# Kernel optimization log

Measured on AMD Instinct MI355X. Metric: run time of the kernel, lower is better.

## Reference

```python
import jax, jax.numpy as jnp
import numpy as np
import math

E_IN, E_OUT = 512, 96
B, QL, PL = 64, 128, 196

def _lin(k, shape):
    fan_in = shape[1]
    bound = 1.0 / math.sqrt(fan_in)
    k1, k2 = jax.random.split(k)
    W = jax.random.uniform(k1, shape, jnp.float32, -bound, bound)
    b = jax.random.uniform(k2, (shape[0],), jnp.float32, -bound, bound)
    return W, b

def setup_inputs() -> dict:
    key = jax.random.key(0)
    ks = jax.random.split(key, 16)
    inp = {
        'z_d_cls': jax.random.normal(ks[0], (B, E_IN), jnp.float32),
        'Z_d_tok': jax.random.normal(ks[1], (B, QL, E_IN), jnp.float32),
        'z_t_cls': jax.random.normal(ks[2], (B, E_IN), jnp.float32),
        'Z_t_tok': jax.random.normal(ks[3], (B, QL, E_IN), jnp.float32),
        'z_v_cls': jax.random.normal(ks[4], (B, E_IN), jnp.float32),
        'Z_v_patch': jax.random.normal(ks[5], (B, PL, E_IN), jnp.float32),
    }
    names = ['t_cls', 'd_cls', 'v_cls', 't_tok', 'v_patch', 'tgl_q', 'tgl_k', 'tgl_v']
    for i, n in enumerate(names):
        W, b = _lin(ks[6 + i], (E_OUT, E_IN))
        inp[f'W_{n}'] = W
        inp[f'b_{n}'] = b
    inp['ln_g'] = jnp.ones((E_OUT,), jnp.float32)
    inp['ln_b'] = jnp.zeros((E_OUT,), jnp.float32)
    return inp

def _l2n(x, eps=1e-6):
    return x / jnp.maximum(jnp.linalg.norm(x, axis=-1, keepdims=True), eps)

def _proj(x, W, b):
    return x @ W.T + b

def _layer_norm(x, g, b, eps=1e-5):
    mu = jnp.mean(x, axis=-1, keepdims=True)
    var = jnp.mean((x - mu) ** 2, axis=-1, keepdims=True)
    return (x - mu) / jnp.sqrt(var + eps) * g + b

def reference(z_d_cls, Z_d_tok, z_t_cls, Z_t_tok, z_v_cls, Z_v_patch,
              W_t_cls, b_t_cls, W_d_cls, b_d_cls, W_v_cls, b_v_cls,
              W_t_tok, b_t_tok, W_v_patch, b_v_patch,
              W_tgl_q, b_tgl_q, W_tgl_k, b_tgl_k, W_tgl_v, b_tgl_v,
              ln_g, ln_b):
    # --- TGG: global-global text/doc cosine sim [B, B]
    t = _l2n(_proj(z_t_cls, W_t_cls, b_t_cls))
    d = _l2n(_proj(z_d_cls, W_d_cls, b_d_cls))
    S_TGG = t @ d.T
    # --- TGL: cross-attention over all batch pairs
    Q = _proj(Z_d_tok, W_tgl_q, b_tgl_q)   # [b, q, h]
    K = _proj(Z_t_tok, W_tgl_k, b_tgl_k)   # [c, k, h]
    V = _proj(Z_t_tok, W_tgl_v, b_tgl_v)   # [c, k, h]
    scores = jnp.einsum('bqh,ckh->bcqk', Q, K) / math.sqrt(E_OUT)
    attn = jax.nn.softmax(scores, axis=-1)
    context = jnp.einsum('bcqk,ckh->bcqh', attn, V).mean(axis=2)  # [b, c, h]
    context = _layer_norm(context, ln_g, ln_b)
    S_TGL = jnp.einsum('ih,ijh->ij', d, _l2n(context))
    S_TIB = 0.5 * (S_TGG + S_TGL)
    # --- CGG: global-global text/vision cosine sim
    v = _l2n(_proj(z_v_cls, W_v_cls, b_v_cls))
    S_CGG = t @ v.T
    # --- CLL: token-patch max similarity
    t_tok = _l2n(_proj(Z_t_tok, W_t_tok, b_t_tok))        # [b, t, h]
    v_pat = _l2n(_proj(Z_v_patch, W_v_patch, b_v_patch))  # [c, p, h]
    sim = jnp.einsum('bth,cph->bctp', t_tok, v_pat)
    S_CLL = sim.max(axis=(-1, -2))
    S_CAB = 0.5 * (S_CGG + S_CLL)
    return S_TIB + S_CAB
```

## Files before the change

kernel.cpp:

```cpp
#include <hip/hip_runtime.h>
#include <hip/hip_bf16.h>
#include <math.h>

typedef __bf16 bf16;
typedef __attribute__((ext_vector_type(8))) __bf16 bf16x8;
typedef __attribute__((ext_vector_type(4))) float f32x4;
typedef __attribute__((ext_vector_type(4))) unsigned int uint4v;

#define MFMA16(a, b, c) __builtin_amdgcn_mfma_f32_16x16x32_bf16(a, b, c, 0, 0, 0)

#define QSCALE 0.14724450f

__device__ inline bf16x8 cvt8(const float* p) {
    f32x4 lo = *(const f32x4*)p;
    f32x4 hi = *(const f32x4*)(p + 4);
    bf16x8 r;
    r[0] = (bf16)lo[0]; r[1] = (bf16)lo[1]; r[2] = (bf16)lo[2]; r[3] = (bf16)lo[3];
    r[4] = (bf16)hi[0]; r[5] = (bf16)hi[1]; r[6] = (bf16)hi[2]; r[7] = (bf16)hi[3];
    return r;
}


struct WPtrs { const float* W[8]; };

__global__ __launch_bounds__(256) void cvtw_kernel(WPtrs wp, bf16* __restrict__ Wb) {
    int j   = blockIdx.x / 48;
    int blk = blockIdx.x - j * 48;
    int idx = (blk * 256 + threadIdx.x) * 4;
    f32x4 v = *(const f32x4*)(wp.W[j] + idx);
    bf16* dst = Wb + j * 49152 + idx;
    dst[0] = (bf16)v[0]; dst[1] = (bf16)v[1]; dst[2] = (bf16)v[2]; dst[3] = (bf16)v[3];
}


struct ProjParams {
    const float* src[8];
    const float* B[8];
    void* dst[8];
    const bf16* Wb;
};

__global__ __launch_bounds__(128, 4) void proj_kernel(ProjParams p) {
    int g   = blockIdx.x;
    int tid = threadIdx.x;
    int nh = tid >> 6, lane = tid & 63;
    int m = lane & 15, quad = lane >> 4;

    int job = 0, base = 0;
    if (g >= 2)    { job = 1; base = 2; }
    if (g >= 4)    { job = 2; base = 4; }
    if (g >= 6)    { job = 3; base = 6; }
    if (g >= 262)  { job = 4; base = 262; }
    if (g >= 518)  { job = 5; base = 518; }
    if (g >= 774)  { job = 6; base = 774; }
    if (g >= 1030) { job = 7; base = 1030; }
    int r0 = (g - base) << 5;

    const float* X  = p.src[job];
    const bf16*  wb = p.Wb + job * 49152 + (size_t)(nh * 48 + m) * 512 + quad * 8;
    const float* x0 = X + (size_t)(r0 + m) * 512 + quad * 8;
    const float* x1 = x0 + 16 * 512;

    f32x4 acc[2][3] = {};
    #pragma unroll 4
    for (int kk = 0; kk < 512; kk += 32) {
        bf16x8 a0 = cvt8(x0 + kk);
        bf16x8 a1 = cvt8(x1 + kk);
        #pragma unroll
        for (int nt = 0; nt < 3; nt++) {
            bf16x8 b = *(const bf16x8*)(wb + nt * 8192 + kk);
            acc[0][nt] = MFMA16(a0, b, acc[0][nt]);
            acc[1][nt] = MFMA16(a1, b, acc[1][nt]);
        }
    }
    const float* Bv = p.B[job];
    #pragma unroll
    for (int t2 = 0; t2 < 2; t2++)
        #pragma unroll
        for (int nt = 0; nt < 3; nt++) {
            float bb = Bv[nh * 48 + nt * 16 + m];
            acc[t2][nt][0] += bb; acc[t2][nt][1] += bb;
            acc[t2][nt][2] += bb; acc[t2][nt][3] += bb;
        }

    bool norm = (job < 3) || (job >= 6);
    __shared__ float sx[2][2][16];
    if (norm) {
        float ss[2][4];
        #pragma unroll
        for (int t2 = 0; t2 < 2; t2++)
            #pragma unroll
            for (int r = 0; r < 4; r++) {
                float s = 0.0f;
                #pragma unroll
                for (int nt = 0; nt < 3; nt++) s += acc[t2][nt][r] * acc[t2][nt][r];
                s += __shfl_xor(s, 1); s += __shfl_xor(s, 2);
                s += __shfl_xor(s, 4); s += __shfl_xor(s, 8);
                ss[t2][r] = s;
            }
        if (m == 0) {
            #pragma unroll
            for (int t2 = 0; t2 < 2; t2++)
                #pragma unroll
                for (int r = 0; r < 4; r++)
                    sx[nh][t2][quad * 4 + r] = ss[t2][r];
        }
        __syncthreads();
        #pragma unroll
        for (int t2 = 0; t2 < 2; t2++)
            #pragma unroll
            for (int r = 0; r < 4; r++) {
                float tot = ss[t2][r] + sx[1 - nh][t2][quad * 4 + r];
                float inv = 1.0f / fmaxf(sqrtf(tot), 1e-6f);
                #pragma unroll
                for (int nt = 0; nt < 3; nt++) acc[t2][nt][r] *= inv;
            }
    } else if (job == 3) {
        #pragma unroll
        for (int t2 = 0; t2 < 2; t2++)
            #pragma unroll
            for (int nt = 0; nt < 3; nt++) {
                acc[t2][nt][0] *= QSCALE; acc[t2][nt][1] *= QSCALE;
                acc[t2][nt][2] *= QSCALE; acc[t2][nt][3] *= QSCALE;
            }
    }
    if (job < 3) {
        float* dst = (float*)p.dst[job];
        #pragma unroll
        for (int t2 = 0; t2 < 2; t2++)
            #pragma unroll
            for (int r = 0; r < 4; r++)
                #pragma unroll
                for (int nt = 0; nt < 3; nt++)
                    dst[(size_t)(r0 + t2 * 16 + quad * 4 + r) * 96 + nh * 48 + nt * 16 + m] = acc[t2][nt][r];
    } else {
        bf16* dst = (bf16*)p.dst[job];
        #pragma unroll
        for (int t2 = 0; t2 < 2; t2++)
            #pragma unroll
            for (int r = 0; r < 4; r++)
                #pragma unroll
                for (int nt = 0; nt < 3; nt++)
                    dst[(size_t)(r0 + t2 * 16 + quad * 4 + r) * 96 + nh * 48 + nt * 16 + m] = (bf16)acc[t2][nt][r];
    }
}


__global__ __launch_bounds__(256) void attn_kernel(
    const bf16* __restrict__ Qg, const bf16* __restrict__ Kg, const bf16* __restrict__ Vg,
    const float* __restrict__ dvec, const float* __restrict__ ln_g, const float* __restrict__ ln_b,
    float* __restrict__ S_TGL)
{
    int pr = blockIdx.x;
    int b = pr >> 6, c = pr & 63;
    int tid = threadIdx.x, lane = tid & 63, w = tid >> 6;
    int m = lane & 15, quad = lane >> 4;
    const bf16* Q = Qg + (size_t)b * (128 * 96);
    const bf16* K = Kg + (size_t)c * (128 * 96);
    const bf16* V = Vg + (size_t)c * (128 * 96);

    f32x4 acc[2][8] = {};
    #pragma unroll
    for (int kk = 0; kk < 96; kk += 32) {
        bf16x8 a0 = *(const bf16x8*)(Q + (size_t)(w * 32 + m) * 96 + kk + quad * 8);
        bf16x8 a1 = *(const bf16x8*)(Q + (size_t)(w * 32 + 16 + m) * 96 + kk + quad * 8);
        #pragma unroll
        for (int nt = 0; nt < 8; nt++) {
            bf16x8 bb = *(const bf16x8*)(K + (size_t)(nt * 16 + m) * 96 + kk + quad * 8);
            acc[0][nt] = MFMA16(a0, bb, acc[0][nt]);
            acc[1][nt] = MFMA16(a1, bb, acc[1][nt]);
        }
    }
    float wpart[8];
    #pragma unroll
    for (int nt = 0; nt < 8; nt++) wpart[nt] = 0.0f;
    #pragma unroll
    for (int mt = 0; mt < 2; mt++) {
        #pragma unroll
        for (int r = 0; r < 4; r++) {
            float tv[8]; float s = 0.0f;
            #pragma unroll
            for (int nt = 0; nt < 8; nt++) { tv[nt] = exp2f(acc[mt][nt][r]); s += tv[nt]; }
            s += __shfl_xor(s, 1); s += __shfl_xor(s, 2);
            s += __shfl_xor(s, 4); s += __shfl_xor(s, 8);
            float inv = 1.0f / s;
            #pragma unroll
            for (int nt = 0; nt < 8; nt++) wpart[nt] += tv[nt] * inv;
        }
    }
    #pragma unroll
    for (int nt = 0; nt < 8; nt++) {
        wpart[nt] += __shfl_xor(wpart[nt], 16);
        wpart[nt] += __shfl_xor(wpart[nt], 32);
    }
    __shared__ float wsum4[4][128];
    __shared__ float wk[128];
    __shared__ float ctxp[4][96];
    __shared__ float ctx[96];
    if (lane < 16) {
        #pragma unroll
        for (int nt = 0; nt < 8; nt++) wsum4[w][nt * 16 + lane] = wpart[nt];
    }
    __syncthreads();
    if (tid < 128) wk[tid] = wsum4[0][tid] + wsum4[1][tid] + wsum4[2][tid] + wsum4[3][tid];
    __syncthreads();
    {
        float c0 = 0.0f, c1 = 0.0f;
        if (lane < 48) {
            #pragma unroll 4
            for (int r = 0; r < 32; r++) {
                int k = w * 32 + r;
                unsigned u = *(const unsigned*)(V + (size_t)k * 96 + lane * 2);
                float lo = __uint_as_float(u << 16);
                float hi = __uint_as_float(u & 0xffff0000u);
                float wkk = wk[k];
                c0 += wkk * lo; c1 += wkk * hi;
            }
            ctxp[w][lane * 2]     = c0;
            ctxp[w][lane * 2 + 1] = c1;
        }
    }
    __syncthreads();
    if (tid < 96) ctx[tid] = (ctxp[0][tid] + ctxp[1][tid] + ctxp[2][tid] + ctxp[3][tid]) * (1.0f / 128.0f);
    __syncthreads();
    if (w == 0) {
        float x0 = ctx[lane];
        float x1 = (lane < 32) ? ctx[64 + lane] : 0.0f;
        float s = x0 + x1;
        #pragma unroll
        for (int d = 1; d < 64; d <<= 1) s += __shfl_xor(s, d);
        float mean = s * (1.0f / 96.0f);
        float e0 = x0 - mean;
        float e1 = (lane < 32) ? (x1 - mean) : 0.0f;
        float q = e0 * e0 + e1 * e1;
        #pragma unroll
        for (int d = 1; d < 64; d <<= 1) q += __shfl_xor(q, d);
        float rstd = rsqrtf(q * (1.0f / 96.0f) + 1e-5f);
        float y0 = e0 * rstd * ln_g[lane] + ln_b[lane];
        float y1 = 0.0f;
        if (lane < 32) y1 = e1 * rstd * ln_g[64 + lane] + ln_b[64 + lane];
        const float* db = dvec + b * 96;
        float dot = y0 * db[lane] + ((lane < 32) ? y1 * db[64 + lane] : 0.0f);
        float ssq = y0 * y0 + y1 * y1;
        #pragma unroll
        for (int d = 1; d < 64; d <<= 1) { dot += __shfl_xor(dot, d); ssq += __shfl_xor(ssq, d); }
        if (lane == 0) S_TGL[pr] = dot / fmaxf(sqrtf(ssq), 1e-6f);
    }
}


__global__ __launch_bounds__(256) void cll_kernel(
    const bf16* __restrict__ Tt, const bf16* __restrict__ Vp, float* __restrict__ S_CLL)
{
    int c = blockIdx.x >> 3, bg = blockIdx.x & 7;
    int tid = threadIdx.x, lane = tid & 63, w = tid >> 6;
    int m = lane & 15, quad = lane >> 4;
    const bf16* P = Vp + (size_t)c * (196 * 96);

    __shared__ __align__(16) bf16 Plds[196 * 104];
    __shared__ float red[8][4];
    for (int ch = tid; ch < 2352; ch += 256) {
        int row = ch / 12, seg = ch - row * 12;
        *(uint4v*)(Plds + row * 104 + seg * 8) = *(const uint4v*)(P + ch * 8);
    }
    int rofs[13];
    #pragma unroll
    for (int nt = 0; nt < 13; nt++) {
        int r = nt * 16 + m; if (r > 195) r = 195;
        rofs[nt] = r * 104;
    }
    __syncthreads();

    for (int bi = 0; bi < 8; bi++) {
        const bf16* T = Tt + (size_t)(bg * 8 + bi) * (128 * 96);
        f32x4 acc[2][13] = {};
        #pragma unroll
        for (int kk = 0; kk < 96; kk += 32) {
            bf16x8 a0 = *(const bf16x8*)(T + (size_t)(w * 32 + m) * 96 + kk + quad * 8);
            bf16x8 a1 = *(const bf16x8*)(T + (size_t)(w * 32 + 16 + m) * 96 + kk + quad * 8);
            #pragma unroll
            for (int nt = 0; nt < 13; nt++) {
                bf16x8 bb = *(const bf16x8*)(Plds + rofs[nt] + kk + quad * 8);
                acc[0][nt] = MFMA16(a0, bb, acc[0][nt]);
                acc[1][nt] = MFMA16(a1, bb, acc[1][nt]);
            }
        }
        float mx = -3.4e38f;
        #pragma unroll
        for (int mt = 0; mt < 2; mt++)
            #pragma unroll
            for (int nt = 0; nt < 13; nt++)
                #pragma unroll
                for (int r = 0; r < 4; r++) mx = fmaxf(mx, acc[mt][nt][r]);
        #pragma unroll
        for (int d = 1; d < 64; d <<= 1) mx = fmaxf(mx, __shfl_xor(mx, d));
        if (lane == 0) red[bi][w] = mx;
    }
    __syncthreads();
    if (tid < 8)
        S_CLL[(size_t)(bg * 8 + tid) * 64 + c] =
            fmaxf(fmaxf(red[tid][0], red[tid][1]), fmaxf(red[tid][2], red[tid][3]));
}


__global__ __launch_bounds__(64) void final_kernel(
    const float* __restrict__ t, const float* __restrict__ d, const float* __restrict__ v,
    const float* __restrict__ S_TGL, const float* __restrict__ S_CLL, float* __restrict__ out)
{
    int i = blockIdx.x, j = threadIdx.x;
    __shared__ float ti[96];
    if (j < 64) ti[j] = t[i * 96 + j];
    if (j < 32) ti[64 + j] = t[i * 96 + 64 + j];
    __syncthreads();
    float tg = 0.0f, cg = 0.0f;
    const float* dj = d + j * 96;
    const float* vj = v + j * 96;
    #pragma unroll 8
    for (int h = 0; h < 96; h++) { float th = ti[h]; tg += th * dj[h]; cg += th * vj[h]; }
    float res = 0.5f * (tg + S_TGL[i * 64 + j]) + 0.5f * (cg + S_CLL[i * 64 + j]);
    out[i * 64 + j] = res;
}


extern "C" void kernel_launch(void* const* d_in, const int* in_sizes, int n_in,
                              void* d_out, int out_size, void* d_ws, size_t ws_size,
                              hipStream_t stream)
{
    (void)in_sizes; (void)n_in; (void)out_size; (void)ws_size;
    char* ws = (char*)d_ws;
    float* t     = (float*)(ws + 0);
    float* d     = (float*)(ws + 24576);
    float* v     = (float*)(ws + 49152);
    float* S_TGL = (float*)(ws + 73728);
    float* S_CLL = (float*)(ws + 90112);
    bf16* Wb = (bf16*)(ws + 106496);
    bf16* Qb = (bf16*)(ws + 892928);
    bf16* Kb = (bf16*)(ws + 892928 + 1572864);
    bf16* Vb = (bf16*)(ws + 892928 + 2 * 1572864);
    bf16* Tt = (bf16*)(ws + 892928 + 3 * 1572864);
    bf16* Vp = (bf16*)(ws + 892928 + 4 * 1572864);

    WPtrs wp;
    wp.W[0] = (const float*)d_in[6];
    wp.W[1] = (const float*)d_in[8];
    wp.W[2] = (const float*)d_in[10];
    wp.W[3] = (const float*)d_in[16];
    wp.W[4] = (const float*)d_in[18];
    wp.W[5] = (const float*)d_in[20];
    wp.W[6] = (const float*)d_in[12];
    wp.W[7] = (const float*)d_in[14];
    hipLaunchKernelGGL(cvtw_kernel, dim3(384), dim3(256), 0, stream, wp, Wb);

    ProjParams pp;
    pp.Wb = Wb;
    pp.src[0] = (const float*)d_in[2];  pp.B[0] = (const float*)d_in[7];  pp.dst[0] = t;
    pp.src[1] = (const float*)d_in[0];  pp.B[1] = (const float*)d_in[9];  pp.dst[1] = d;
    pp.src[2] = (const float*)d_in[4];  pp.B[2] = (const float*)d_in[11]; pp.dst[2] = v;
    pp.src[3] = (const float*)d_in[1];  pp.B[3] = (const float*)d_in[17]; pp.dst[3] = Qb;
    pp.src[4] = (const float*)d_in[3];  pp.B[4] = (const float*)d_in[19]; pp.dst[4] = Kb;
    pp.src[5] = (const float*)d_in[3];  pp.B[5] = (const float*)d_in[21]; pp.dst[5] = Vb;
    pp.src[6] = (const float*)d_in[3];  pp.B[6] = (const float*)d_in[13]; pp.dst[6] = Tt;
    pp.src[7] = (const float*)d_in[5];  pp.B[7] = (const float*)d_in[15]; pp.dst[7] = Vp;
    hipLaunchKernelGGL(proj_kernel, dim3(1422), dim3(128), 0, stream, pp);

    hipLaunchKernelGGL(attn_kernel, dim3(4096), dim3(256), 0, stream,
                       (const bf16*)Qb, (const bf16*)Kb, (const bf16*)Vb,
                       (const float*)d, (const float*)d_in[22], (const float*)d_in[23], S_TGL);
    hipLaunchKernelGGL(cll_kernel, dim3(512), dim3(256), 0, stream,
                       (const bf16*)Tt, (const bf16*)Vp, S_CLL);
    hipLaunchKernelGGL(final_kernel, dim3(64), dim3(64), 0, stream,
                       (const float*)t, (const float*)d, (const float*)v,
                       (const float*)S_TGL, (const float*)S_CLL, (float*)d_out);
}
```

Before: 261.1 us.

## Stage K in LDS for attention and move LayerNorm epilogue to separate kernel

The attention kernel now copies each K tile into padded shared memory before the QK MFMA loop, so all four waves read K from LDS instead of re-reading it from global memory. The per-pair LayerNorm, normalisation and dot-product tail is taken out of the attention kernel. The attention kernel writes the raw context vector to a new workspace buffer, and a wider epilogue kernel (one wave per pair) does the LayerNorm and combines the TGG, CGG and CLL terms. The cost is an extra global round trip of the 4096x96 context and an added barrier plus 26KB of LDS per attention block, which may reduce occupancy.

```diff
diff --git a/kernel.cpp b/kernel.cpp
--- a/kernel.cpp
+++ b/kernel.cpp
@@ -4,6 +4,7 @@
 
 typedef __bf16 bf16;
 typedef __attribute__((ext_vector_type(8))) __bf16 bf16x8;
+typedef __attribute__((ext_vector_type(2))) float f32x2;
 typedef __attribute__((ext_vector_type(4))) float f32x4;
 typedef __attribute__((ext_vector_type(4))) unsigned int uint4v;
 
@@ -148,8 +149,7 @@
 
 __global__ __launch_bounds__(256) void attn_kernel(
     const bf16* __restrict__ Qg, const bf16* __restrict__ Kg, const bf16* __restrict__ Vg,
-    const float* __restrict__ dvec, const float* __restrict__ ln_g, const float* __restrict__ ln_b,
-    float* __restrict__ S_TGL)
+    float* __restrict__ Ctx)
 {
     int pr = blockIdx.x;
     int b = pr >> 6, c = pr & 63;
@@ -159,6 +159,15 @@
     const bf16* K = Kg + (size_t)c * (128 * 96);
     const bf16* V = Vg + (size_t)c * (128 * 96);
 
+    __shared__ __align__(16) bf16 Klds[128 * 104];
+    #pragma unroll
+    for (int it = 0; it < 6; it++) {
+        int ch = it * 256 + tid;
+        int row = ch / 12, seg = ch - row * 12;
+        *(uint4v*)(Klds + row * 104 + seg * 8) = *(const uint4v*)(K + ch * 8);
+    }
+    __syncthreads();
+
     f32x4 acc[2][8] = {};
     #pragma unroll
     for (int kk = 0; kk < 96; kk += 32) {
@@ -166,7 +175,7 @@
         bf16x8 a1 = *(const bf16x8*)(Q + (size_t)(w * 32 + 16 + m) * 96 + kk + quad * 8);
         #pragma unroll
         for (int nt = 0; nt < 8; nt++) {
-            bf16x8 bb = *(const bf16x8*)(K + (size_t)(nt * 16 + m) * 96 + kk + quad * 8);
+            bf16x8 bb = *(const bf16x8*)(Klds + (nt * 16 + m) * 104 + kk + quad * 8);
             acc[0][nt] = MFMA16(a0, bb, acc[0][nt]);
             acc[1][nt] = MFMA16(a1, bb, acc[1][nt]);
         }
@@ -196,7 +205,6 @@
     __shared__ float wsum4[4][128];
     __shared__ float wk[128];
     __shared__ float ctxp[4][96];
-    __shared__ float ctx[96];
     if (lane < 16) {
         #pragma unroll
         for (int nt = 0; nt < 8; nt++) wsum4[w][nt * 16 + lane] = wpart[nt];
@@ -221,31 +229,9 @@
         }
     }
     __syncthreads();
-    if (tid < 96) ctx[tid] = (ctxp[0][tid] + ctxp[1][tid] + ctxp[2][tid] + ctxp[3][tid]) * (1.0f / 128.0f);
-    __syncthreads();
-    if (w == 0) {
-        float x0 = ctx[lane];
-        float x1 = (lane < 32) ? ctx[64 + lane] : 0.0f;
-        float s = x0 + x1;
-        #pragma unroll
-        for (int d = 1; d < 64; d <<= 1) s += __shfl_xor(s, d);
-        float mean = s * (1.0f / 96.0f);
-        float e0 = x0 - mean;
-        float e1 = (lane < 32) ? (x1 - mean) : 0.0f;
-        float q = e0 * e0 + e1 * e1;
-        #pragma unroll
-        for (int d = 1; d < 64; d <<= 1) q += __shfl_xor(q, d);
-        float rstd = rsqrtf(q * (1.0f / 96.0f) + 1e-5f);
-        float y0 = e0 * rstd * ln_g[lane] + ln_b[lane];
-        float y1 = 0.0f;
-        if (lane < 32) y1 = e1 * rstd * ln_g[64 + lane] + ln_b[64 + lane];
-        const float* db = dvec + b * 96;
-        float dot = y0 * db[lane] + ((lane < 32) ? y1 * db[64 + lane] : 0.0f);
-        float ssq = y0 * y0 + y1 * y1;
-        #pragma unroll
-        for (int d = 1; d < 64; d <<= 1) { dot += __shfl_xor(dot, d); ssq += __shfl_xor(ssq, d); }
-        if (lane == 0) S_TGL[pr] = dot / fmaxf(sqrtf(ssq), 1e-6f);
-    }
+    if (tid < 96)
+        Ctx[(size_t)pr * 96 + tid] =
+            (ctxp[0][tid] + ctxp[1][tid] + ctxp[2][tid] + ctxp[3][tid]) * (1.0f / 128.0f);
 }
 
 
@@ -303,22 +289,57 @@
 }
 
 
-__global__ __launch_bounds__(64) void final_kernel(
-    const float* __restrict__ t, const float* __restrict__ d, const float* __restrict__ v,
-    const float* __restrict__ S_TGL, const float* __restrict__ S_CLL, float* __restrict__ out)
+__global__ __launch_bounds__(256) void epi_kernel(
+    const float* __restrict__ Ctx, const float* __restrict__ t, const float* __restrict__ d,
+    const float* __restrict__ v, const float* __restrict__ S_CLL,
+    const float* __restrict__ ln_g, const float* __restrict__ ln_b,
+    float* __restrict__ out)
 {
-    int i = blockIdx.x, j = threadIdx.x;
-    __shared__ float ti[96];
-    if (j < 64) ti[j] = t[i * 96 + j];
-    if (j < 32) ti[64 + j] = t[i * 96 + 64 + j];
-    __syncthreads();
-    float tg = 0.0f, cg = 0.0f;
-    const float* dj = d + j * 96;
-    const float* vj = v + j * 96;
-    #pragma unroll 8
-    for (int h = 0; h < 96; h++) { float th = ti[h]; tg += th * dj[h]; cg += th * vj[h]; }
-    float res = 0.5f * (tg + S_TGL[i * 64 + j]) + 0.5f * (cg + S_CLL[i * 64 + j]);
-    out[i * 64 + j] = res;
+    int pr = blockIdx.x * 4 + (threadIdx.x >> 6);
+    int lane = threadIdx.x & 63;
+    int i = pr >> 6, j = pr & 63;
+    bool act = lane < 48;
+
+    float c0 = 0, c1 = 0, t0 = 0, t1 = 0;
+    float dj0 = 0, dj1 = 0, di0 = 0, di1 = 0, v0 = 0, v1 = 0, g0 = 0, g1 = 0, bb0 = 0, bb1 = 0;
+    if (act) {
+        f32x2 cc  = *(const f32x2*)(Ctx + (size_t)pr * 96 + lane * 2);
+        f32x2 tt  = *(const f32x2*)(t + i * 96 + lane * 2);
+        f32x2 ddj = *(const f32x2*)(d + j * 96 + lane * 2);
+        f32x2 ddi = *(const f32x2*)(d + i * 96 + lane * 2);
+        f32x2 vv  = *(const f32x2*)(v + j * 96 + lane * 2);
+        f32x2 gg  = *(const f32x2*)(ln_g + lane * 2);
+        f32x2 bbv = *(const f32x2*)(ln_b + lane * 2);
+        c0 = cc[0]; c1 = cc[1]; t0 = tt[0]; t1 = tt[1];
+        dj0 = ddj[0]; dj1 = ddj[1]; di0 = ddi[0]; di1 = ddi[1];
+        v0 = vv[0]; v1 = vv[1];
+        g0 = gg[0]; g1 = gg[1]; bb0 = bbv[0]; bb1 = bbv[1];
+    }
+    float s = c0 + c1;
+    #pragma unroll
+    for (int k = 1; k < 64; k <<= 1) s += __shfl_xor(s, k);
+    float mean = s * (1.0f / 96.0f);
+    float e0 = act ? (c0 - mean) : 0.0f;
+    float e1 = act ? (c1 - mean) : 0.0f;
+    float q = e0 * e0 + e1 * e1;
+    #pragma unroll
+    for (int k = 1; k < 64; k <<= 1) q += __shfl_xor(q, k);
+    float rstd = rsqrtf(q * (1.0f / 96.0f) + 1e-5f);
+    float y0 = act ? (e0 * rstd * g0 + bb0) : 0.0f;
+    float y1 = act ? (e1 * rstd * g1 + bb1) : 0.0f;
+    float dot = y0 * di0 + y1 * di1;
+    float ssq = y0 * y0 + y1 * y1;
+    float tg  = t0 * dj0 + t1 * dj1;
+    float cg  = t0 * v0 + t1 * v1;
+    #pragma unroll
+    for (int k = 1; k < 64; k <<= 1) {
+        dot += __shfl_xor(dot, k); ssq += __shfl_xor(ssq, k);
+        tg  += __shfl_xor(tg, k);  cg  += __shfl_xor(cg, k);
+    }
+    if (lane == 0) {
+        float stgl = dot / fmaxf(sqrtf(ssq), 1e-6f);
+        out[pr] = 0.5f * (tg + stgl) + 0.5f * (cg + S_CLL[pr]);
+    }
 }
 
 
@@ -331,7 +352,6 @@
     float* t     = (float*)(ws + 0);
     float* d     = (float*)(ws + 24576);
     float* v     = (float*)(ws + 49152);
-    float* S_TGL = (float*)(ws + 73728);
     float* S_CLL = (float*)(ws + 90112);
     bf16* Wb = (bf16*)(ws + 106496);
     bf16* Qb = (bf16*)(ws + 892928);
@@ -339,6 +359,7 @@
     bf16* Vb = (bf16*)(ws + 892928 + 2 * 1572864);
     bf16* Tt = (bf16*)(ws + 892928 + 3 * 1572864);
     bf16* Vp = (bf16*)(ws + 892928 + 4 * 1572864);
+    float* Ctx = (float*)(ws + 892928 + 4 * 1572864 + 2408448);
 
     WPtrs wp;
     wp.W[0] = (const float*)d_in[6];
@@ -364,11 +385,11 @@
     hipLaunchKernelGGL(proj_kernel, dim3(1422), dim3(128), 0, stream, pp);
 
     hipLaunchKernelGGL(attn_kernel, dim3(4096), dim3(256), 0, stream,
-                       (const bf16*)Qb, (const bf16*)Kb, (const bf16*)Vb,
-                       (const float*)d, (const float*)d_in[22], (const float*)d_in[23], S_TGL);
+                       (const bf16*)Qb, (const bf16*)Kb, (const bf16*)Vb, Ctx);
     hipLaunchKernelGGL(cll_kernel, dim3(512), dim3(256), 0, stream,
                        (const bf16*)Tt, (const bf16*)Vp, S_CLL);
-    hipLaunchKernelGGL(final_kernel, dim3(64), dim3(64), 0, stream,
-                       (const float*)t, (const float*)d, (const float*)v,
-                       (const float*)S_TGL, (const float*)S_CLL, (float*)d_out);
-}
+    hipLaunchKernelGGL(epi_kernel, dim3(1024), dim3(256), 0, stream,
+                       (const float*)Ctx, (const float*)t, (const float*)d, (const float*)v,
+                       (const float*)S_CLL, (const float*)d_in[22], (const float*)d_in[23],
+                       (float*)d_out);
+}
```

New measurement: 240.7 us. -7.8%, faster.
